# Kernel tuning notes

Measured on AMD Instinct MI355X. Metric: run time of the kernel, lower is better.

## Reference

```python
import jax, jax.numpy as jnp
import numpy as np

N_STATIONS = 100000
N_TIME = 365
N_NEIGHBORS = 5
SMOOTHING = 0.1


def setup_inputs() -> dict:
    key = jax.random.key(0)
    k = jax.random.split(key, 6)
    N, T, K = N_STATIONS, N_TIME, N_NEIGHBORS
    time_vector = jnp.arange(T, dtype=jnp.float32) / 365.25  # years
    constant_offset = jax.random.normal(k[0], (N,), jnp.float32) * 10.0
    linear_trend = jax.random.normal(k[1], (N,), jnp.float32) * 5.0  # mm/yr (ps00_rates buffer)
    seasonal_amplitudes = jax.random.uniform(k[2], (N, 4), jnp.float32) * 6.0
    seasonal_phases = jax.random.uniform(k[3], (N, 4), jnp.float32) * (2.0 * np.pi)
    neighbor_indices = jax.random.randint(k[4], (N, K), 0, N)
    w = jax.random.uniform(k[5], (N, K), jnp.float32) + 1e-3
    neighbor_weights = w / jnp.sum(w, axis=1, keepdims=True)  # row-normalized, like exp-dist weights
    periods = jnp.array([0.25, 0.5, 1.0, 2.0], dtype=jnp.float32)
    return {
        'time_vector': time_vector,
        'constant_offset': constant_offset,
        'linear_trend': linear_trend,
        'seasonal_amplitudes': seasonal_amplitudes,
        'seasonal_phases': seasonal_phases,
        'neighbor_weights': neighbor_weights,
        'periods': periods,
        'neighbor_indices': neighbor_indices,
    }


def _smooth(p, neighbor_indices, neighbor_weights):
    # p: [N, 4]; vectorized version of per-station loop: gather + weighted mean
    nb = p[neighbor_indices]                                   # [N, K, 4]
    avg = jnp.einsum('nkf,nk->nf', nb, neighbor_weights)       # [N, 4]
    return (1.0 - SMOOTHING) * p + SMOOTHING * avg


def reference(time_vector, constant_offset, linear_trend, seasonal_amplitudes,
              seasonal_phases, neighbor_weights, periods, neighbor_indices):
    amps = _smooth(seasonal_amplitudes, neighbor_indices, neighbor_weights)   # [N, 4]
    phs = _smooth(seasonal_phases, neighbor_indices, neighbor_weights)        # [N, 4]
    t = time_vector[None, :]                                                  # [1, T]
    signals = constant_offset[:, None] + linear_trend[:, None] * t           # [N, T]
    two_pi = jnp.float32(2.0 * np.pi)
    for f in range(4):  # fixed small set of seasonal periods
        freq = 1.0 / periods[f]
        signals = signals + amps[:, f:f + 1] * jnp.sin(two_pi * freq * t + phs[:, f:f + 1])
    return signals
```

## Files before the change

### kernel.cpp

```cpp
#include <hip/hip_runtime.h>
#include <math.h>

typedef float f32x2 __attribute__((ext_vector_type(2)));

#define TWO_PI 6.283185307179586f
#define SMOOTH 0.1f
#define SPW 8
#define WAVES 4
#define BLOCK 256
#define SPB (SPW * WAVES)
#define NPAIR 3

__device__ __forceinline__ f32x2 sp2(float x) { f32x2 r; r.x = x; r.y = x; return r; }
__device__ __forceinline__ void store8(float* p, f32x2 v) { __builtin_memcpy(p, &v, 8); }
__device__ __forceinline__ float rlane(float v, int l) {
    return __uint_as_float((unsigned)__builtin_amdgcn_readlane((int)__float_as_uint(v), l));
}

__global__ __launch_bounds__(BLOCK) void fused_v5(
    const float* __restrict__ time_vector,
    const float* __restrict__ constant_offset,
    const float* __restrict__ linear_trend,
    const float* __restrict__ amps,
    const float* __restrict__ phs,
    const float* __restrict__ wgt,
    const float* __restrict__ periods,
    const int*   __restrict__ nbidx,
    float* __restrict__ out,
    int N, int T, int K)
{
    const int tid   = threadIdx.x;
    const int wave  = tid >> 6;
    const int lane  = tid & 63;
    const int wbase = blockIdx.x * SPB + wave * SPW;

    if (wbase >= N) return;
    int send = N - wbase; if (send > SPW) send = SPW;

    int sid = wbase + (lane & (SPW - 1));
    if (sid >= N) sid = N - 1;

    float4 a = reinterpret_cast<const float4*>(amps)[sid];
    float4 p = reinterpret_cast<const float4*>(phs)[sid];

    int   nb[5]; float w[5];
    __builtin_memcpy(nb, nbidx + (size_t)sid * K, 5 * sizeof(int));
    __builtin_memcpy(w,  wgt   + (size_t)sid * K, 5 * sizeof(float));

    float av0 = 0.f, av1 = 0.f, av2 = 0.f, av3 = 0.f;
    float pv0 = 0.f, pv1 = 0.f, pv2 = 0.f, pv3 = 0.f;
    #pragma unroll
    for (int k = 0; k < 5; ++k) {
        float4 na = reinterpret_cast<const float4*>(amps)[nb[k]];
        float4 np = reinterpret_cast<const float4*>(phs)[nb[k]];
        av0 += w[k] * na.x; av1 += w[k] * na.y; av2 += w[k] * na.z; av3 += w[k] * na.w;
        pv0 += w[k] * np.x; pv1 += w[k] * np.y; pv2 += w[k] * np.z; pv3 += w[k] * np.w;
    }
    float sa0 = (1.0f - SMOOTH) * a.x + SMOOTH * av0;
    float sa1 = (1.0f - SMOOTH) * a.y + SMOOTH * av1;
    float sa2 = (1.0f - SMOOTH) * a.z + SMOOTH * av2;
    float sa3 = (1.0f - SMOOTH) * a.w + SMOOTH * av3;
    float sp0 = (1.0f - SMOOTH) * p.x + SMOOTH * pv0;
    float sp1 = (1.0f - SMOOTH) * p.y + SMOOTH * pv1;
    float sp2v = (1.0f - SMOOTH) * p.z + SMOOTH * pv2;
    float sp3 = (1.0f - SMOOTH) * p.w + SMOOTH * pv3;

    float cc = constant_offset[sid];
    float cm = linear_trend[sid];
    float cA0 = sa0 * __cosf(sp0),  cB0 = sa0 * __sinf(sp0);
    float cA1 = sa1 * __cosf(sp1),  cB1 = sa1 * __sinf(sp1);
    float cA2 = sa2 * __cosf(sp2v), cB2 = sa2 * __sinf(sp2v);
    float cA3 = sa3 * __cosf(sp3),  cB3 = sa3 * __sinf(sp3);

    const float w0 = TWO_PI / periods[0];
    const float w1 = TWO_PI / periods[1];
    const float w2 = TWO_PI / periods[2];
    const float w3 = TWO_PI / periods[3];

    f32x2 tv[NPAIR];
    f32x2 bs[NPAIR][4], bc[NPAIR][4];
    bool full[NPAIR], any[NPAIR];
    const int t0 = 2 * lane;

    #pragma unroll
    for (int q = 0; q < NPAIR; ++q) {
        const int t = t0 + 128 * q;
        const bool v0 = (t < T), v1 = (t + 1 < T);
        any[q] = v0; full[q] = v1;
        float ta = v0 ? time_vector[t]     : 0.f;
        float tb = v1 ? time_vector[t + 1] : 0.f;
        f32x2 tvp; tvp.x = ta; tvp.y = tb;
        tv[q] = tvp;
        #pragma unroll
        for (int f = 0; f < 4; ++f) {
            const float wf = (f == 0) ? w0 : (f == 1) ? w1 : (f == 2) ? w2 : w3;
            f32x2 s, c;
            s.x = __sinf(wf * ta); s.y = __sinf(wf * tb);
            c.x = __cosf(wf * ta); c.y = __cosf(wf * tb);
            bs[q][f] = s; bc[q][f] = c;
        }
    }

    float* obase = out + (size_t)wbase * T;

    #pragma unroll
    for (int j = 0; j < SPW; ++j) {
        if (j >= send) break;
        float sc  = rlane(cc,  j), sm  = rlane(cm,  j);
        float sA0 = rlane(cA0, j), sB0 = rlane(cB0, j);
        float sA1 = rlane(cA1, j), sB1 = rlane(cB1, j);
        float sA2 = rlane(cA2, j), sB2 = rlane(cB2, j);
        float sA3 = rlane(cA3, j), sB3 = rlane(cB3, j);
        float* orow = obase + (size_t)j * T;

        #pragma unroll
        for (int q = 0; q < NPAIR; ++q) {
            f32x2 sig = sp2(sc) + sp2(sm) * tv[q];
            sig += sp2(sA0) * bs[q][0] + sp2(sB0) * bc[q][0];
            sig += sp2(sA1) * bs[q][1] + sp2(sB1) * bc[q][1];
            sig += sp2(sA2) * bs[q][2] + sp2(sB2) * bc[q][2];
            sig += sp2(sA3) * bs[q][3] + sp2(sB3) * bc[q][3];
            const int t = t0 + 128 * q;
            if (full[q])      store8(orow + t, sig);
            else if (any[q])  orow[t] = sig.x;
        }
    }
}

extern "C" void kernel_launch(void* const* d_in, const int* in_sizes, int n_in,
                              void* d_out, int out_size, void* d_ws, size_t ws_size,
                              hipStream_t stream)
{
    const float* time_vector     = (const float*)d_in[0];
    const float* constant_offset = (const float*)d_in[1];
    const float* linear_trend    = (const float*)d_in[2];
    const float* amps            = (const float*)d_in[3];
    const float* phs             = (const float*)d_in[4];
    const float* wgt             = (const float*)d_in[5];
    const float* periods         = (const float*)d_in[6];
    const int*   nbidx           = (const int*)d_in[7];

    int T = in_sizes[0];
    int N = in_sizes[1];
    int K = in_sizes[5] / N;
    float* out = (float*)d_out;

    int grid = (N + SPB - 1) / SPB;
    fused_v5<<<grid, BLOCK, 0, stream>>>(
        time_vector, constant_offset, linear_trend, amps, phs, wgt,
        periods, nbidx, out, N, T, K);
}
```

Baseline: 40.29 us.

## Stage output rows in LDS and write them out as contiguous float4 stores

Each wave now writes four station rows into shared memory, then copies that contiguous block to global memory with 16-byte vector stores. This replaces per-lane 8-byte strided row stores. The aim is wider, fully contiguous global writes for the write-bandwidth-bound output. In exchange it adds shared-memory traffic, wave barriers and about 23 KB of LDS per block, which may limit occupancy. A tail path keeps direct stores for partial waves.

```diff
diff --git a/kernel.cpp b/kernel.cpp
--- a/kernel.cpp
+++ b/kernel.cpp
@@ -10,14 +10,14 @@
 #define BLOCK 256
 #define SPB (SPW * WAVES)
 #define NPAIR 3
+#define HROWS 4
 
 __device__ __forceinline__ f32x2 sp2(float x) { f32x2 r; r.x = x; r.y = x; return r; }
-__device__ __forceinline__ void store8(float* p, f32x2 v) { __builtin_memcpy(p, &v, 8); }
 __device__ __forceinline__ float rlane(float v, int l) {
     return __uint_as_float((unsigned)__builtin_amdgcn_readlane((int)__float_as_uint(v), l));
 }
 
-__global__ __launch_bounds__(BLOCK) void fused_v5(
+__global__ __launch_bounds__(BLOCK) void fused_v7(
     const float* __restrict__ time_vector,
     const float* __restrict__ constant_offset,
     const float* __restrict__ linear_trend,
@@ -29,6 +29,8 @@
     float* __restrict__ out,
     int N, int T, int K)
 {
+    extern __shared__ float lds[];
+
     const int tid   = threadIdx.x;
     const int wave  = tid >> 6;
     const int lane  = tid & 63;
@@ -101,28 +103,66 @@
         }
     }
 
-    float* obase = out + (size_t)wbase * T;
+    float* wlds = lds + (size_t)wave * HROWS * T;
 
-    #pragma unroll
-    for (int j = 0; j < SPW; ++j) {
-        if (j >= send) break;
-        float sc  = rlane(cc,  j), sm  = rlane(cm,  j);
-        float sA0 = rlane(cA0, j), sB0 = rlane(cB0, j);
-        float sA1 = rlane(cA1, j), sB1 = rlane(cB1, j);
-        float sA2 = rlane(cA2, j), sB2 = rlane(cB2, j);
-        float sA3 = rlane(cA3, j), sB3 = rlane(cB3, j);
-        float* orow = obase + (size_t)j * T;
+    if (send == SPW) {
+        #pragma unroll
+        for (int half = 0; half < 2; ++half) {
+            #pragma unroll
+            for (int j4 = 0; j4 < HROWS; ++j4) {
+                const int j = half * HROWS + j4;
+                float sc  = rlane(cc,  j), sm  = rlane(cm,  j);
+                float sA0 = rlane(cA0, j), sB0 = rlane(cB0, j);
+                float sA1 = rlane(cA1, j), sB1 = rlane(cB1, j);
+                float sA2 = rlane(cA2, j), sB2 = rlane(cB2, j);
+                float sA3 = rlane(cA3, j), sB3 = rlane(cB3, j);
+                float* lrow = wlds + j4 * T;
 
-        #pragma unroll
-        for (int q = 0; q < NPAIR; ++q) {
-            f32x2 sig = sp2(sc) + sp2(sm) * tv[q];
-            sig += sp2(sA0) * bs[q][0] + sp2(sB0) * bc[q][0];
-            sig += sp2(sA1) * bs[q][1] + sp2(sB1) * bc[q][1];
-            sig += sp2(sA2) * bs[q][2] + sp2(sB2) * bc[q][2];
-            sig += sp2(sA3) * bs[q][3] + sp2(sB3) * bc[q][3];
-            const int t = t0 + 128 * q;
-            if (full[q])      store8(orow + t, sig);
-            else if (any[q])  orow[t] = sig.x;
+                #pragma unroll
+                for (int q = 0; q < NPAIR; ++q) {
+                    f32x2 sig = sp2(sc) + sp2(sm) * tv[q];
+                    sig += sp2(sA0) * bs[q][0] + sp2(sB0) * bc[q][0];
+                    sig += sp2(sA1) * bs[q][1] + sp2(sB1) * bc[q][1];
+                    sig += sp2(sA2) * bs[q][2] + sp2(sB2) * bc[q][2];
+                    sig += sp2(sA3) * bs[q][3] + sp2(sB3) * bc[q][3];
+                    const int t = t0 + 128 * q;
+                    if (full[q]) { lrow[t] = sig.x; lrow[t + 1] = sig.y; }
+                    else if (any[q]) { lrow[t] = sig.x; }
+                }
+            }
+            __builtin_amdgcn_sched_barrier(0);
+            __builtin_amdgcn_wave_barrier();
+
+            const float4* src = reinterpret_cast<const float4*>(wlds);
+            float4* dst = reinterpret_cast<float4*>(
+                out + ((size_t)wbase + half * HROWS) * T);
+            const int nch = T;
+            for (int it = lane; it < nch; it += 64)
+                dst[it] = src[it];
+
+            __builtin_amdgcn_sched_barrier(0);
+            __builtin_amdgcn_wave_barrier();
+        }
+    } else {
+        float* obase = out + (size_t)wbase * T;
+        for (int j = 0; j < send; ++j) {
+            float sc  = rlane(cc,  j), sm  = rlane(cm,  j);
+            float sA0 = rlane(cA0, j), sB0 = rlane(cB0, j);
+            float sA1 = rlane(cA1, j), sB1 = rlane(cB1, j);
+            float sA2 = rlane(cA2, j), sB2 = rlane(cB2, j);
+            float sA3 = rlane(cA3, j), sB3 = rlane(cB3, j);
+            float* orow = obase + (size_t)j * T;
+            #pragma unroll
+            for (int q = 0; q < NPAIR; ++q) {
+                f32x2 sig = sp2(sc) + sp2(sm) * tv[q];
+                sig += sp2(sA0) * bs[q][0] + sp2(sB0) * bc[q][0];
+                sig += sp2(sA1) * bs[q][1] + sp2(sB1) * bc[q][1];
+                sig += sp2(sA2) * bs[q][2] + sp2(sB2) * bc[q][2];
+                sig += sp2(sA3) * bs[q][3] + sp2(sB3) * bc[q][3];
+                const int t = t0 + 128 * q;
+                if (full[q]) { orow[t] = sig.x; orow[t + 1] = sig.y; }
+                else if (any[q]) { orow[t] = sig.x; }
+            }
         }
     }
 }
@@ -146,7 +186,8 @@
     float* out = (float*)d_out;
 
     int grid = (N + SPB - 1) / SPB;
-    fused_v5<<<grid, BLOCK, 0, stream>>>(
+    size_t shmem = (size_t)WAVES * HROWS * T * sizeof(float);
+    fused_v7<<<grid, BLOCK, shmem, stream>>>(
         time_vector, constant_offset, linear_trend, amps, phs, wgt,
         periods, nbidx, out, N, T, K);
 }
```

New measurement: 40.41 us. About the same (+0.3%).

## Split into coefficient/basis-table precompute kernel and a streaming writer kernel

Applied to the files above, without the earlier changes.

Splits the fused kernel into two launches. The first computes the smoothed per-station harmonic coefficients into a workspace buffer, along with a shared sin/cos basis table over time. The second kernel only loads these and streams the output rows. This removes the redundant per-wave transcendental basis evaluation and the gather latency from the write-bound kernel. In exchange it adds a second launch, extra global traffic for the coefficient buffer, and a serialization point between the kernels.

```diff
diff --git a/kernel.cpp b/kernel.cpp
--- a/kernel.cpp
+++ b/kernel.cpp
@@ -10,14 +10,17 @@
 #define BLOCK 256
 #define SPB (SPW * WAVES)
 #define NPAIR 3
+#define TP_ROWS 192
+#define TP_BYTES (TP_ROWS * 16 * 4)
 
 __device__ __forceinline__ f32x2 sp2(float x) { f32x2 r; r.x = x; r.y = x; return r; }
+__device__ __forceinline__ f32x2 mk2(float a, float b) { f32x2 r; r.x = a; r.y = b; return r; }
 __device__ __forceinline__ void store8(float* p, f32x2 v) { __builtin_memcpy(p, &v, 8); }
 __device__ __forceinline__ float rlane(float v, int l) {
     return __uint_as_float((unsigned)__builtin_amdgcn_readlane((int)__float_as_uint(v), l));
 }
 
-__global__ __launch_bounds__(BLOCK) void fused_v5(
+__global__ void coef_table_kernel(
     const float* __restrict__ time_vector,
     const float* __restrict__ constant_offset,
     const float* __restrict__ linear_trend,
@@ -26,8 +29,68 @@
     const float* __restrict__ wgt,
     const float* __restrict__ periods,
     const int*   __restrict__ nbidx,
+    float* __restrict__ tableP,
+    float* __restrict__ coef,
+    int N, int T, int K)
+{
+    int i = blockIdx.x * blockDim.x + threadIdx.x;
+
+    if (i < T) {
+        float tv = time_vector[i];
+        const int p = i >> 1, o = i & 1;
+        float* row = tableP + p * 16;
+        #pragma unroll
+        for (int f = 0; f < 4; ++f) {
+            float ang = (TWO_PI / periods[f]) * tv;
+            row[2 * f + o]     = __sinf(ang);
+            row[8 + 2 * f + o] = __cosf(ang);
+        }
+    }
+
+    if (i < N) {
+        float4 a = reinterpret_cast<const float4*>(amps)[i];
+        float4 p = reinterpret_cast<const float4*>(phs)[i];
+
+        int   nb[5]; float w[5];
+        __builtin_memcpy(nb, nbidx + (size_t)i * K, 5 * sizeof(int));
+        __builtin_memcpy(w,  wgt   + (size_t)i * K, 5 * sizeof(float));
+
+        float av0 = 0.f, av1 = 0.f, av2 = 0.f, av3 = 0.f;
+        float pv0 = 0.f, pv1 = 0.f, pv2 = 0.f, pv3 = 0.f;
+        #pragma unroll
+        for (int k = 0; k < 5; ++k) {
+            float4 na = reinterpret_cast<const float4*>(amps)[nb[k]];
+            float4 np = reinterpret_cast<const float4*>(phs)[nb[k]];
+            av0 += w[k] * na.x; av1 += w[k] * na.y; av2 += w[k] * na.z; av3 += w[k] * na.w;
+            pv0 += w[k] * np.x; pv1 += w[k] * np.y; pv2 += w[k] * np.z; pv3 += w[k] * np.w;
+        }
+        float sa0 = (1.0f - SMOOTH) * a.x + SMOOTH * av0;
+        float sa1 = (1.0f - SMOOTH) * a.y + SMOOTH * av1;
+        float sa2 = (1.0f - SMOOTH) * a.z + SMOOTH * av2;
+        float sa3 = (1.0f - SMOOTH) * a.w + SMOOTH * av3;
+        float sp0 = (1.0f - SMOOTH) * p.x + SMOOTH * pv0;
+        float sp1 = (1.0f - SMOOTH) * p.y + SMOOTH * pv1;
+        float sp2 = (1.0f - SMOOTH) * p.z + SMOOTH * pv2;
+        float sp3 = (1.0f - SMOOTH) * p.w + SMOOTH * pv3;
+
+        float4 vA, vB, vC;
+        vA.x = constant_offset[i]; vA.y = linear_trend[i];
+        vA.z = sa0 * __cosf(sp0);  vA.w = sa0 * __sinf(sp0);
+        vB.x = sa1 * __cosf(sp1);  vB.y = sa1 * __sinf(sp1);
+        vB.z = sa2 * __cosf(sp2);  vB.w = sa2 * __sinf(sp2);
+        vC.x = sa3 * __cosf(sp3);  vC.y = sa3 * __sinf(sp3);
+        vC.z = 0.f; vC.w = 0.f;
+        float4* cp = reinterpret_cast<float4*>(coef + (size_t)i * 12);
+        cp[0] = vA; cp[1] = vB; cp[2] = vC;
+    }
+}
+
+__global__ __launch_bounds__(BLOCK) void writer_kernel(
+    const float* __restrict__ time_vector,
+    const float* __restrict__ tableP,
+    const float* __restrict__ coef,
     float* __restrict__ out,
-    int N, int T, int K)
+    int N, int T)
 {
     const int tid   = threadIdx.x;
     const int wave  = tid >> 6;
@@ -39,48 +102,15 @@
 
     int sid = wbase + (lane & (SPW - 1));
     if (sid >= N) sid = N - 1;
+    const float4* cp = reinterpret_cast<const float4*>(coef + (size_t)sid * 12);
+    float4 k0 = cp[0];
+    float4 k1 = cp[1];
+    float4 k2 = cp[2];
 
-    float4 a = reinterpret_cast<const float4*>(amps)[sid];
-    float4 p = reinterpret_cast<const float4*>(phs)[sid];
-
-    int   nb[5]; float w[5];
-    __builtin_memcpy(nb, nbidx + (size_t)sid * K, 5 * sizeof(int));
-    __builtin_memcpy(w,  wgt   + (size_t)sid * K, 5 * sizeof(float));
-
-    float av0 = 0.f, av1 = 0.f, av2 = 0.f, av3 = 0.f;
-    float pv0 = 0.f, pv1 = 0.f, pv2 = 0.f, pv3 = 0.f;
-    #pragma unroll
-    for (int k = 0; k < 5; ++k) {
-        float4 na = reinterpret_cast<const float4*>(amps)[nb[k]];
-        float4 np = reinterpret_cast<const float4*>(phs)[nb[k]];
-        av0 += w[k] * na.x; av1 += w[k] * na.y; av2 += w[k] * na.z; av3 += w[k] * na.w;
-        pv0 += w[k] * np.x; pv1 += w[k] * np.y; pv2 += w[k] * np.z; pv3 += w[k] * np.w;
-    }
-    float sa0 = (1.0f - SMOOTH) * a.x + SMOOTH * av0;
-    float sa1 = (1.0f - SMOOTH) * a.y + SMOOTH * av1;
-    float sa2 = (1.0f - SMOOTH) * a.z + SMOOTH * av2;
-    float sa3 = (1.0f - SMOOTH) * a.w + SMOOTH * av3;
-    float sp0 = (1.0f - SMOOTH) * p.x + SMOOTH * pv0;
-    float sp1 = (1.0f - SMOOTH) * p.y + SMOOTH * pv1;
-    float sp2v = (1.0f - SMOOTH) * p.z + SMOOTH * pv2;
-    float sp3 = (1.0f - SMOOTH) * p.w + SMOOTH * pv3;
-
-    float cc = constant_offset[sid];
-    float cm = linear_trend[sid];
-    float cA0 = sa0 * __cosf(sp0),  cB0 = sa0 * __sinf(sp0);
-    float cA1 = sa1 * __cosf(sp1),  cB1 = sa1 * __sinf(sp1);
-    float cA2 = sa2 * __cosf(sp2v), cB2 = sa2 * __sinf(sp2v);
-    float cA3 = sa3 * __cosf(sp3),  cB3 = sa3 * __sinf(sp3);
-
-    const float w0 = TWO_PI / periods[0];
-    const float w1 = TWO_PI / periods[1];
-    const float w2 = TWO_PI / periods[2];
-    const float w3 = TWO_PI / periods[3];
-
+    const int t0 = 2 * lane;
     f32x2 tv[NPAIR];
     f32x2 bs[NPAIR][4], bc[NPAIR][4];
     bool full[NPAIR], any[NPAIR];
-    const int t0 = 2 * lane;
 
     #pragma unroll
     for (int q = 0; q < NPAIR; ++q) {
@@ -89,16 +119,17 @@
         any[q] = v0; full[q] = v1;
         float ta = v0 ? time_vector[t]     : 0.f;
         float tb = v1 ? time_vector[t + 1] : 0.f;
-        f32x2 tvp; tvp.x = ta; tvp.y = tb;
-        tv[q] = tvp;
-        #pragma unroll
-        for (int f = 0; f < 4; ++f) {
-            const float wf = (f == 0) ? w0 : (f == 1) ? w1 : (f == 2) ? w2 : w3;
-            f32x2 s, c;
-            s.x = __sinf(wf * ta); s.y = __sinf(wf * tb);
-            c.x = __cosf(wf * ta); c.y = __cosf(wf * tb);
-            bs[q][f] = s; bc[q][f] = c;
-        }
+        tv[q] = mk2(ta, tb);
+
+        const float4* rp = reinterpret_cast<const float4*>(tableP + (size_t)(lane + 64 * q) * 16);
+        float4 r0 = rp[0];
+        float4 r1 = rp[1];
+        float4 r2 = rp[2];
+        float4 r3 = rp[3];
+        bs[q][0] = mk2(r0.x, r0.y); bs[q][1] = mk2(r0.z, r0.w);
+        bs[q][2] = mk2(r1.x, r1.y); bs[q][3] = mk2(r1.z, r1.w);
+        bc[q][0] = mk2(r2.x, r2.y); bc[q][1] = mk2(r2.z, r2.w);
+        bc[q][2] = mk2(r3.x, r3.y); bc[q][3] = mk2(r3.z, r3.w);
     }
 
     float* obase = out + (size_t)wbase * T;
@@ -106,11 +137,11 @@
     #pragma unroll
     for (int j = 0; j < SPW; ++j) {
         if (j >= send) break;
-        float sc  = rlane(cc,  j), sm  = rlane(cm,  j);
-        float sA0 = rlane(cA0, j), sB0 = rlane(cB0, j);
-        float sA1 = rlane(cA1, j), sB1 = rlane(cB1, j);
-        float sA2 = rlane(cA2, j), sB2 = rlane(cB2, j);
-        float sA3 = rlane(cA3, j), sB3 = rlane(cB3, j);
+        float sc  = rlane(k0.x, j), sm  = rlane(k0.y, j);
+        float sA0 = rlane(k0.z, j), sB0 = rlane(k0.w, j);
+        float sA1 = rlane(k1.x, j), sB1 = rlane(k1.y, j);
+        float sA2 = rlane(k1.z, j), sB2 = rlane(k1.w, j);
+        float sA3 = rlane(k2.x, j), sB3 = rlane(k2.y, j);
         float* orow = obase + (size_t)j * T;
 
         #pragma unroll
@@ -145,8 +176,17 @@
     int K = in_sizes[5] / N;
     float* out = (float*)d_out;
 
-    int grid = (N + SPB - 1) / SPB;
-    fused_v5<<<grid, BLOCK, 0, stream>>>(
+    float* tableP = (float*)d_ws;
+    float* coef   = (float*)((char*)d_ws + TP_BYTES);
+
+    int threads = 256;
+    int workA = (N > T) ? N : T;
+    int gridA = (workA + threads - 1) / threads;
+    coef_table_kernel<<<gridA, threads, 0, stream>>>(
         time_vector, constant_offset, linear_trend, amps, phs, wgt,
-        periods, nbidx, out, N, T, K);
+        periods, nbidx, tableP, coef, N, T, K);
+
+    int gridW = (N + SPB - 1) / SPB;
+    writer_kernel<<<gridW, BLOCK, 0, stream>>>(
+        time_vector, tableP, coef, out, N, T);
 }
```

After: 42.08 us. 1.04x slower.
